# Optimization experiments

Hardware: AMD Instinct MI355X
Metric: run time of the kernel (lower is better)

The kernel has to match this reference:

```python
import jax, jax.numpy as jnp
import numpy as np

B, N, K, D, H, T = 32, 4096, 8, 256, 4, 3
DH = D // H
SCALE = DH ** -0.5
EPS = 1e-8
HID = 256


def layernorm(x, w, b, eps=1e-5):
    m = jnp.mean(x, axis=-1, keepdims=True)
    v = jnp.var(x, axis=-1, keepdims=True)
    return (x - m) * jax.lax.rsqrt(v + eps) * w + b


def setup_inputs() -> dict:
    key = jax.random.key(0)
    ks = jax.random.split(key, 20)
    p = 0.02
    inp = {
        "x": jax.random.normal(ks[0], (B, N, D), jnp.float32),
        "noise": jax.random.normal(ks[1], (B, K, D), jnp.float32),
        "mu": jax.random.normal(ks[2], (1, 1, D), jnp.float32),
        "log_sigma": jax.random.normal(ks[3], (1, 1, D), jnp.float32) * p,
        "norm_in_w": jnp.ones((D,), jnp.float32), "norm_in_b": jnp.zeros((D,), jnp.float32),
        "norm_slot_w": jnp.ones((D,), jnp.float32), "norm_slot_b": jnp.zeros((D,), jnp.float32),
        "norm_mlp_w": jnp.ones((D,), jnp.float32), "norm_mlp_b": jnp.zeros((D,), jnp.float32),
        "Wq": jax.random.normal(ks[4], (D, D), jnp.float32) * p,
        "Wk": jax.random.normal(ks[5], (D, D), jnp.float32) * p,
        "Wv": jax.random.normal(ks[6], (D, D), jnp.float32) * p,
        "Wo": jax.random.normal(ks[7], (D, D), jnp.float32) * p,
        "gru_Wih": jax.random.normal(ks[8], (3 * D, D), jnp.float32) * p,
        "gru_Whh": jax.random.normal(ks[9], (3 * D, D), jnp.float32) * p,
        "gru_bih": jnp.zeros((3 * D,), jnp.float32),
        "gru_bhh": jnp.zeros((3 * D,), jnp.float32),
        "mlp_W1": jax.random.normal(ks[10], (HID, D), jnp.float32) * p,
        "mlp_b1": jnp.zeros((HID,), jnp.float32),
        "mlp_W2": jax.random.normal(ks[11], (D, HID), jnp.float32) * p,
        "mlp_b2": jnp.zeros((D,), jnp.float32),
    }
    return inp


def _split(t):
    # [b, n, D] -> [b, H, n, d_h]
    b, n, _ = t.shape
    return t.reshape(b, n, H, DH).transpose(0, 2, 1, 3)


def _merge(t):
    # [b, H, n, d_h] -> [b, n, D]
    b, h, n, d = t.shape
    return t.transpose(0, 2, 1, 3).reshape(b, n, h * d)


def _step(slots, k_feat, v_feat, p):
    b, k, d = slots.shape
    q = _split(layernorm(slots, p["norm_slot_w"], p["norm_slot_b"]) @ p["Wq"].T)
    dots = jnp.einsum("bhkd,bhnd->bhkn", q, k_feat) * SCALE
    attn = jax.nn.softmax(dots, axis=2)              # softmax over slot (query) axis
    attn = attn / (jnp.sum(attn, axis=-1, keepdims=True) + EPS)  # renorm over keys
    upd = _merge(jnp.einsum("bhkn,bhnd->bhkd", attn, v_feat)) @ p["Wo"].T
    # GRUCell(update, slots)
    gi = upd @ p["gru_Wih"].T + p["gru_bih"]
    gh = slots @ p["gru_Whh"].T + p["gru_bhh"]
    i_r, i_z, i_n = jnp.split(gi, 3, axis=-1)
    h_r, h_z, h_n = jnp.split(gh, 3, axis=-1)
    r = jax.nn.sigmoid(i_r + h_r)
    z = jax.nn.sigmoid(i_z + h_z)
    n = jnp.tanh(i_n + r * h_n)
    slots = (1.0 - z) * n + z * slots
    h1 = jax.nn.relu(layernorm(slots, p["norm_mlp_w"], p["norm_mlp_b"]) @ p["mlp_W1"].T + p["mlp_b1"])
    return slots + h1 @ p["mlp_W2"].T + p["mlp_b2"]


def reference(x, noise, mu, log_sigma, norm_in_w, norm_in_b, norm_slot_w, norm_slot_b,
              norm_mlp_w, norm_mlp_b, Wq, Wk, Wv, Wo, gru_Wih, gru_Whh, gru_bih, gru_bhh,
              mlp_W1, mlp_b1, mlp_W2, mlp_b2):
    p = dict(norm_slot_w=norm_slot_w, norm_slot_b=norm_slot_b, norm_mlp_w=norm_mlp_w,
             norm_mlp_b=norm_mlp_b, Wq=Wq, Wo=Wo, gru_Wih=gru_Wih, gru_Whh=gru_Whh,
             gru_bih=gru_bih, gru_bhh=gru_bhh, mlp_W1=mlp_W1, mlp_b1=mlp_b1,
             mlp_W2=mlp_W2, mlp_b2=mlp_b2)
    slots = mu + jnp.exp(log_sigma) * noise          # [B, K, D]
    xn = layernorm(x, norm_in_w, norm_in_b)
    k_feat = _split(xn @ Wk.T)                       # [B, H, N, d_h]
    v_feat = _split(xn @ Wv.T)
    for _ in range(T):
        slots = _step(slots, k_feat, v_feat, p)
    return slots
```

## Files before the change

kernel.cpp:

```cpp
#include <hip/hip_runtime.h>
#include <stdint.h>

typedef unsigned short ushort_t;
typedef __attribute__((ext_vector_type(8))) short bfrag;
typedef __attribute__((ext_vector_type(4))) float ffrag;

#define B_  32
#define K_  8
#define N_  4096
#define D_  256
#define H_  4
#define DH_ 64

__device__ __forceinline__ ushort_t f2bf(float f) {
  unsigned int u = __builtin_bit_cast(unsigned int, f);
  u += 0x7FFFu + ((u >> 16) & 1u);
  return (ushort_t)(u >> 16);
}

__global__ __launch_bounds__(256) void k_prep_wkv(const float* __restrict__ Wk, const float* __restrict__ Wv,
                                                  const float* __restrict__ lnw, const float* __restrict__ lnb,
                                                  ushort_t* __restrict__ wkv,
                                                  float* __restrict__ c1, float* __restrict__ c2) {
  int n = blockIdx.x;
  int i = threadIdx.x;
  float wv = (n < 256) ? Wk[n*256 + i] : Wv[(n-256)*256 + i];
  float wp = lnw[i] * wv;
  wkv[n*256 + i] = f2bf(wp);
  float p1 = wp, p2 = lnb[i] * wv;
  #pragma unroll
  for (int off = 32; off >= 1; off >>= 1) { p1 += __shfl_xor(p1, off); p2 += __shfl_xor(p2, off); }
  __shared__ float r1[4], r2[4];
  int w = threadIdx.x >> 6;
  if ((threadIdx.x & 63) == 0) { r1[w] = p1; r2[w] = p2; }
  __syncthreads();
  if (threadIdx.x == 0) { c1[n] = r1[0]+r1[1]+r1[2]+r1[3]; c2[n] = r2[0]+r2[1]+r2[2]+r2[3]; }
}

__global__ __launch_bounds__(256) void k_prep_wf(const float* __restrict__ Wih, const float* __restrict__ Wo,
                                                 float* __restrict__ Wf) {
  int j = blockIdx.x;
  int i = threadIdx.x;
  __shared__ float row[256];
  row[i] = Wih[j*256 + i];
  __syncthreads();
  float acc = 0.f;
  #pragma unroll 8
  for (int t = 0; t < 256; ++t) acc += row[t] * Wo[t*256 + i];
  Wf[j*256 + i] = acc;
}

__device__ __forceinline__ void row_ln_256(float (*S)[256], float (*L)[256],
                                           const float* __restrict__ w, const float* __restrict__ b, int t) {
  int k = t >> 5, ln = t & 31;
  float s = 0.f, q = 0.f;
  #pragma unroll
  for (int j = 0; j < 8; ++j) { float v = S[k][ln + j*32]; s += v; q += v*v; }
  #pragma unroll
  for (int off = 16; off >= 1; off >>= 1) { s += __shfl_xor(s, off); q += __shfl_xor(q, off); }
  float m = s * (1.f/256.f);
  float rstd = rsqrtf(q * (1.f/256.f) - m*m + 1e-5f);
  #pragma unroll
  for (int j = 0; j < 8; ++j) {
    int c = ln + j*32;
    L[k][c] = (S[k][c] - m) * rstd * w[c] + b[c];
  }
}

__device__ __forceinline__ void qproj(float (*L)[256], const float* __restrict__ Wq,
                                      ushort_t* __restrict__ qbuf, int b, int t) {
  int c = t;
  const float4* Wrow = (const float4*)(Wq + (size_t)c * 256);
  float acc[8];
  #pragma unroll
  for (int k = 0; k < 8; ++k) acc[k] = 0.f;
  for (int i = 0; i < 64; ++i) {
    float4 wv = Wrow[i];
    #pragma unroll
    for (int k = 0; k < 8; ++k) {
      float4 xv = *((const float4*)&L[k][0] + i);
      acc[k] = fmaf(xv.x, wv.x, fmaf(xv.y, wv.y, fmaf(xv.z, wv.z, fmaf(xv.w, wv.w, acc[k]))));
    }
  }
  int h = c >> 6, dh = c & 63;
  ushort_t* dst = qbuf + ((size_t)(b*4 + h) * 16) * 64 + dh;
  #pragma unroll
  for (int k = 0; k < 8; ++k) dst[k*64] = f2bf(acc[k] * 0.125f);
  #pragma unroll
  for (int k = 8; k < 16; ++k) dst[k*64] = 0;
}

__device__ __forceinline__ void row_ln_4x(float (*S)[256], float (*L)[256],
                                          const float* __restrict__ w, const float* __restrict__ b, int t) {
  int k = t >> 6, ln = t & 63;
  float s = 0.f, q = 0.f;
  #pragma unroll
  for (int j = 0; j < 4; ++j) { float v = S[k][ln + j*64]; s += v; q += v*v; }
  #pragma unroll
  for (int off = 32; off >= 1; off >>= 1) { s += __shfl_xor(s, off); q += __shfl_xor(q, off); }
  float m = s * (1.f/256.f);
  float rstd = rsqrtf(q * (1.f/256.f) - m*m + 1e-5f);
  #pragma unroll
  for (int j = 0; j < 4; ++j) {
    int c = ln + j*64;
    L[k][c] = (S[k][c] - m) * rstd * w[c] + b[c];
  }
}

__device__ __forceinline__ void qproj4(float (*L)[256], const float* __restrict__ Wq,
                                       ushort_t* __restrict__ qbuf, int b, int ks0, int t) {
  int c = t;
  const float4* Wrow = (const float4*)(Wq + (size_t)c * 256);
  float acc[4];
  #pragma unroll
  for (int k = 0; k < 4; ++k) acc[k] = 0.f;
  for (int i = 0; i < 64; ++i) {
    float4 wv = Wrow[i];
    #pragma unroll
    for (int k = 0; k < 4; ++k) {
      float4 xv = *((const float4*)&L[k][0] + i);
      acc[k] = fmaf(xv.x, wv.x, fmaf(xv.y, wv.y, fmaf(xv.z, wv.z, fmaf(xv.w, wv.w, acc[k]))));
    }
  }
  int h = c >> 6, dh = c & 63;
  ushort_t* dst = qbuf + ((size_t)(b*4 + h) * 16) * 64 + dh;
  #pragma unroll
  for (int k = 0; k < 4; ++k) dst[(ks0 + k)*64] = f2bf(acc[k] * 0.125f);
  #pragma unroll
  for (int k = 0; k < 4; ++k) dst[(8 + ks0 + k)*64] = 0;
}

__global__ __launch_bounds__(256) void k_init(const float* __restrict__ noise, const float* __restrict__ mu,
                                              const float* __restrict__ lsig, float* __restrict__ slots,
                                              const float* __restrict__ nsw, const float* __restrict__ nsb,
                                              const float* __restrict__ Wq, ushort_t* __restrict__ qbuf) {
  int b = blockIdx.x, t = threadIdx.x;
  __shared__ float S[8][256];
  __shared__ float L[8][256];
  float e = __expf(lsig[t]);
  float m = mu[t];
  #pragma unroll
  for (int k = 0; k < 8; ++k) {
    float v = m + e * noise[((size_t)(b*8+k))*256 + t];
    S[k][t] = v;
    slots[((size_t)(b*8+k))*256 + t] = v;
  }
  __syncthreads();
  row_ln_256(S, L, nsw, nsb, t);
  __syncthreads();
  qproj(L, Wq, qbuf, b, t);
}

__global__ __launch_bounds__(256, 3) void k_gemm(const float* __restrict__ x,
                                                 const ushort_t* __restrict__ wkv,
                                                 const float* __restrict__ c1, const float* __restrict__ c2,
                                                 ushort_t* __restrict__ kf, ushort_t* __restrict__ vfT) {
  int mb = blockIdx.x, cb = blockIdx.y;
  int t = threadIdx.x, w = t >> 6, l = t & 63;
  __shared__ uint4 ldsv[2048];
  char* lds = (char*)ldsv;
  const int m0 = mb * 128, col0 = cb * 128;
  int r0 = t >> 1, half = t & 1;

  float4 xa[4];
  uint4 wb[2];
  float ssum = 0.f, sqsum = 0.f;
  int swzW = ((r0 >> 1) & 3) << 4;

  auto loadA = [&](int s) {
    const float4* src = (const float4*)(x + (size_t)(m0 + r0) * 256 + s*32 + half*16);
    #pragma unroll
    for (int i = 0; i < 4; ++i) xa[i] = src[i];
  };
  auto loadB = [&](int s) {
    const uint4* src = (const uint4*)(wkv + (size_t)(col0 + r0) * 256 + s*32 + half*16);
    wb[0] = src[0]; wb[1] = src[1];
  };
  auto writeA = [&](char* Ab) {
    #pragma unroll
    for (int i = 0; i < 2; ++i) {
      float4 a = xa[2*i], b2 = xa[2*i+1];
      ssum  += a.x + a.y + a.z + a.w + b2.x + b2.y + b2.z + b2.w;
      sqsum += a.x*a.x + a.y*a.y + a.z*a.z + a.w*a.w
             + b2.x*b2.x + b2.y*b2.y + b2.z*b2.z + b2.w*b2.w;
      union { ushort_t us[8]; uint4 v; } u;
      u.us[0]=f2bf(a.x);  u.us[1]=f2bf(a.y);  u.us[2]=f2bf(a.z);  u.us[3]=f2bf(a.w);
      u.us[4]=f2bf(b2.x); u.us[5]=f2bf(b2.y); u.us[6]=f2bf(b2.z); u.us[7]=f2bf(b2.w);
      *(uint4*)(Ab + r0*64 + ((half*32 + i*16) ^ swzW)) = u.v;
    }
  };
  auto writeB = [&](char* Bb) {
    #pragma unroll
    for (int i = 0; i < 2; ++i)
      *(uint4*)(Bb + r0*64 + ((half*32 + i*16) ^ swzW)) = wb[i];
  };

  ffrag acc[4][4];
  #pragma unroll
  for (int i = 0; i < 4; ++i)
    #pragma unroll
    for (int j = 0; j < 4; ++j) acc[i][j] = (ffrag){0.f,0.f,0.f,0.f};

  int wm = w & 1, wn = w >> 1;
  int lrow = l & 15, lkb = ((l >> 4) * 8) * 2;

  loadA(0); loadB(0);
  writeA(lds); writeB(lds + 16384);
  __syncthreads();

  for (int s = 0; s < 8; ++s) {
    char* Ac = lds + ((s & 1) << 13);
    char* Bc = lds + 16384 + ((s & 1) << 13);
    if (s < 7) { loadA(s+1); loadB(s+1); }
    bfrag bfr[4];
    #pragma unroll
    for (int j = 0; j < 4; ++j) {
      int row = wn*64 + j*16 + lrow;
      bfr[j] = *(const bfrag*)(Bc + row*64 + (lkb ^ (((row >> 1) & 3) << 4)));
    }
    #pragma unroll
    for (int i = 0; i < 4; ++i) {
      int row = wm*64 + i*16 + lrow;
      bfrag afr = *(const bfrag*)(Ac + row*64 + (lkb ^ (((row >> 1) & 3) << 4)));
      #pragma unroll
      for (int j = 0; j < 4; ++j)
        acc[i][j] = __builtin_amdgcn_mfma_f32_16x16x32_bf16(afr, bfr[j], acc[i][j], 0, 0, 0);
    }
    if (s < 7) {
      char* An = lds + (((s+1) & 1) << 13);
      char* Bn = lds + 16384 + (((s+1) & 1) << 13);
      writeA(An); writeB(Bn);
    }
    __syncthreads();
  }

  float s2 = ssum  + __shfl_xor(ssum, 1);
  float q2 = sqsum + __shfl_xor(sqsum, 1);
  float* statm = (float*)(lds + 28672);
  float* statr = (float*)(lds + 29184);
  if (half == 0) {
    float mm = s2 * (1.f/256.f);
    statm[r0] = mm;
    statr[r0] = rsqrtf(q2 * (1.f/256.f) - mm*mm + 1e-5f);
  }
  __syncthreads();

  int g = l >> 4, nl = l & 15;
  int b = m0 >> 12, nx0 = m0 & 4095;
  if (cb < 2) {
    for (int p = 0; p < 2; ++p) {
      if (wm == p) {
        #pragma unroll
        for (int i = 0; i < 4; ++i) {
          #pragma unroll
          for (int j = 0; j < 4; ++j) {
            int coll = wn*64 + j*16 + nl;
            float cc1 = c1[col0 + coll], cc2 = c2[col0 + coll];
            #pragma unroll
            for (int r = 0; r < 4; ++r) {
              int ml = i*16 + g*4 + r;
              int mlg = p*64 + ml;
              float val = statr[mlg] * (acc[i][j][r] - statm[mlg] * cc1) + cc2;
              *(ushort_t*)(lds + (ml*136 + coll)*2) = f2bf(val);
            }
          }
        }
      }
      __syncthreads();
      {
        int mloc = t >> 2, hh = (t >> 1) & 1, qq = t & 1;
        int h = cb*2 + hh;
        ushort_t* dst = kf + ((size_t)((b*4 + h)*4096 + nx0 + p*64 + mloc)) * 64 + qq*32;
        const char* srcr = lds + mloc*272 + hh*128 + qq*64;
        #pragma unroll
        for (int jj = 0; jj < 4; ++jj)
          ((uint4*)dst)[jj] = *(const uint4*)(srcr + jj*16);
      }
      __syncthreads();
    }
  } else {
    for (int p = 0; p < 2; ++p) {
      if (wn == p) {
        #pragma unroll
        for (int i = 0; i < 4; ++i) {
          int mlb = wm*64 + i*16 + g*4;
          #pragma unroll
          for (int j = 0; j < 4; ++j) {
            int coll = j*16 + nl;
            int collg = p*64 + coll;
            float cc1 = c1[col0 + collg], cc2 = c2[col0 + collg];
            ushort_t us[4];
            #pragma unroll
            for (int r = 0; r < 4; ++r)
              us[r] = f2bf(statr[mlb+r] * (acc[i][j][r] - statm[mlb+r] * cc1) + cc2);
            *(uint2*)(lds + coll*272 + mlb*2) =
              make_uint2((unsigned)us[0] | ((unsigned)us[1] << 16),
                         (unsigned)us[2] | ((unsigned)us[3] << 16));
          }
        }
      }
      __syncthreads();
      {
        int cl = t >> 2, seg = t & 3;
        int collg = p*64 + cl;
        int h = (cb - 2)*2 + (collg >> 6);
        int dh = collg & 63;
        ushort_t* dst = vfT + ((size_t)((b*4 + h)*64 + dh)) * 4096 + nx0 + seg*32;
        const char* srcr = lds + cl*272 + seg*64;
        #pragma unroll
        for (int jj = 0; jj < 4; ++jj)
          ((uint4*)dst)[jj] = *(const uint4*)(srcr + jj*16);
      }
      __syncthreads();
    }
  }
}

__global__ __launch_bounds__(256, 4) void k_attn(const ushort_t* __restrict__ q, const ushort_t* __restrict__ kf,
                                                 const ushort_t* __restrict__ vfT,
                                                 float* __restrict__ updp, float* __restrict__ asump) {
  int split = blockIdx.x;
  int bh = blockIdx.y;
  int n0 = split * 256;
  int t = threadIdx.x, w = t >> 6, l = t & 63;
  __shared__ uint4 ldsv[640];
  char* lds = (char*)ldsv;
  char* Pl = lds;
  char* Ql = lds + 8192;

  if (t < 128) {
    int k = t >> 3, seg = t & 7;
    uint4 v = *(const uint4*)(q + ((size_t)bh*16 + k) * 64 + seg*8);
    *(uint4*)(Ql + k*128 + ((seg*16) ^ ((k & 7) << 4))) = v;
  }
  *(uint4*)(Pl + 4096 + t*16) = make_uint4(0,0,0,0);
  __syncthreads();

  int g = l >> 4, nl = l & 15, lk = g * 8;
  const ushort_t* kbase = kf + ((size_t)bh*4096 + n0) * 64;

  ffrag dacc[4];
  #pragma unroll
  for (int nt = 0; nt < 4; ++nt) {
    dacc[nt] = (ffrag){0.f,0.f,0.f,0.f};
    int row = w*64 + nt*16 + nl;
    #pragma unroll
    for (int kk = 0; kk < 2; ++kk) {
      bfrag af = *(const bfrag*)(Ql + nl*128 + (((kk*32 + lk)*2) ^ ((nl & 7) << 4)));
      bfrag bf = *(const bfrag*)(kbase + (size_t)row*64 + kk*32 + lk);
      dacc[nt] = __builtin_amdgcn_mfma_f32_16x16x32_bf16(af, bf, dacc[nt], 0, 0, 0);
    }
  }

  float asr0 = 0.f, asr1 = 0.f, asr2 = 0.f, asr3 = 0.f;
  #pragma unroll
  for (int nt = 0; nt < 4; ++nt) {
    float d0 = dacc[nt][0], d1 = dacc[nt][1], d2 = dacc[nt][2], d3 = dacc[nt][3];
    float mx = fmaxf(fmaxf(d0, d1), fmaxf(d2, d3));
    mx = fmaxf(mx, __shfl_xor(mx, 16));
    float p0 = __expf(d0 - mx), p1 = __expf(d1 - mx), p2 = __expf(d2 - mx), p3 = __expf(d3 - mx);
    float sden = p0 + p1 + p2 + p3;
    sden += __shfl_xor(sden, 16);
    float inv = 1.f / sden;
    p0 *= inv; p1 *= inv; p2 *= inv; p3 *= inv;
    if (g < 2) {
      asr0 += p0; asr1 += p1; asr2 += p2; asr3 += p3;
      int n = w*64 + nt*16 + nl;
      int k0 = g*4;
      *(ushort_t*)(Pl + (((k0+0)*512 + n*2) ^ (((k0+0)&7) << 4))) = f2bf(p0);
      *(ushort_t*)(Pl + (((k0+1)*512 + n*2) ^ (((k0+1)&7) << 4))) = f2bf(p1);
      *(ushort_t*)(Pl + (((k0+2)*512 + n*2) ^ (((k0+2)&7) << 4))) = f2bf(p2);
      *(ushort_t*)(Pl + (((k0+3)*512 + n*2) ^ (((k0+3)&7) << 4))) = f2bf(p3);
    }
  }
  #pragma unroll
  for (int off = 8; off >= 1; off >>= 1) {
    asr0 += __shfl_xor(asr0, off); asr1 += __shfl_xor(asr1, off);
    asr2 += __shfl_xor(asr2, off); asr3 += __shfl_xor(asr3, off);
  }
  if (g < 2 && nl == 0) {
    float* dst = asump + (((size_t)bh*16 + split)*4 + w)*8 + g*4;
    dst[0] = asr0; dst[1] = asr1; dst[2] = asr2; dst[3] = asr3;
  }
  __syncthreads();

  const ushort_t* vbase = vfT + ((size_t)bh*64) * 4096 + n0;
  ffrag pacc = (ffrag){0.f,0.f,0.f,0.f};
  int d = w*16 + nl;
  #pragma unroll
  for (int ni = 0; ni < 8; ++ni) {
    int nn = ni * 32;
    bfrag af = *(const bfrag*)(Pl + nl*512 + (((nn + lk)*2) ^ ((nl & 7) << 4)));
    bfrag bf = *(const bfrag*)(vbase + (size_t)d*4096 + nn + lk);
    pacc = __builtin_amdgcn_mfma_f32_16x16x32_bf16(af, bf, pacc, 0, 0, 0);
  }
  if (g < 2) {
    float* dst = updp + (((size_t)bh*16 + split)*8 + g*4)*64 + w*16 + nl;
    #pragma unroll
    for (int r = 0; r < 4; ++r) dst[r*64] = pacc[r];
  }
}

__global__ __launch_bounds__(256) void k_u1(const float* __restrict__ updp, const float* __restrict__ asump,
                                            const float* __restrict__ slots,
                                            const float* __restrict__ Wf, const float* __restrict__ Whh,
                                            const float* __restrict__ bih, const float* __restrict__ bhh,
                                            float* __restrict__ gi, float* __restrict__ gh) {
  int cb = blockIdx.x, b = blockIdx.y, t = threadIdx.x;
  int c = cb * 256 + t;
  bool isGi = (c < 768);
  __shared__ float X[8][256];
  __shared__ float asumS[4][8];
  if (isGi) {
    if (t < 32) {
      int h = t >> 3, kk = t & 7;
      const float* ap = asump + (size_t)(b*4 + h) * 512;
      float a = 0.f;
      #pragma unroll
      for (int s = 0; s < 64; ++s) a += ap[s*8 + kk];
      asumS[h][kk] = a + 1e-8f;
    }
    __syncthreads();
    int h = t >> 6, d = t & 63;
    const float* up = updp + (size_t)(b*4 + h) * 8192 + d;
    #pragma unroll
    for (int k = 0; k < 8; ++k) {
      float u = 0.f;
      #pragma unroll
      for (int s = 0; s < 16; ++s) u += up[s*512 + k*64];
      X[k][t] = u / asumS[h][k];
    }
  } else {
    #pragma unroll
    for (int k = 0; k < 8; ++k) X[k][t] = slots[((size_t)(b*8+k))*256 + t];
  }
  __syncthreads();
  int cc = isGi ? c : (c - 768);
  const float* Wrow = (isGi ? Wf : Whh) + (size_t)cc * 256;
  float bias = isGi ? bih[cc] : bhh[cc];
  float acc[8];
  #pragma unroll
  for (int k = 0; k < 8; ++k) acc[k] = bias;
  for (int i = 0; i < 64; ++i) {
    float4 wv = ((const float4*)Wrow)[i];
    #pragma unroll
    for (int k = 0; k < 8; ++k) {
      float4 xv = *((const float4*)&X[k][0] + i);
      acc[k] = fmaf(xv.x, wv.x, fmaf(xv.y, wv.y, fmaf(xv.z, wv.z, fmaf(xv.w, wv.w, acc[k]))));
    }
  }
  float* dst = isGi ? gi : gh;
  #pragma unroll
  for (int k = 0; k < 8; ++k) dst[((size_t)(b*8+k))*768 + cc] = acc[k];
}

__global__ __launch_bounds__(256) void k_u2(const float* __restrict__ gi, const float* __restrict__ gh,
                                            const float* __restrict__ slots_in, float* __restrict__ slots_out,
                                            const float* __restrict__ nmw, const float* __restrict__ nmb,
                                            const float* __restrict__ W1, const float* __restrict__ b1,
                                            const float* __restrict__ W2, const float* __restrict__ b2,
                                            const float* __restrict__ nsw, const float* __restrict__ nsb,
                                            const float* __restrict__ Wq, ushort_t* __restrict__ qbuf, int do_q) {
  int bid = blockIdx.x;
  int b = bid >> 1, ks0 = (bid & 1) * 4;
  int t = threadIdx.x;
  __shared__ float S[4][256];
  __shared__ float L[4][256];
  __shared__ float H1[4][256];
  #pragma unroll
  for (int k = 0; k < 4; ++k) {
    int slot = b*8 + ks0 + k;
    size_t gb = (size_t)slot * 768;
    float ir = gi[gb + t],        hr = gh[gb + t];
    float iz = gi[gb + 256 + t],  hz = gh[gb + 256 + t];
    float in_ = gi[gb + 512 + t], hn = gh[gb + 512 + t];
    float r = 1.f / (1.f + __expf(-(ir + hr)));
    float z = 1.f / (1.f + __expf(-(iz + hz)));
    float a = in_ + r * hn;
    float e2 = __expf(-2.f * fabsf(a));
    float nn = (1.f - e2) / (1.f + e2);
    nn = copysignf(nn, a);
    S[k][t] = (1.f - z) * nn + z * slots_in[(size_t)slot * 256 + t];
  }
  __syncthreads();
  row_ln_4x(S, L, nmw, nmb, t);
  __syncthreads();
  {
    const float4* Wrow = (const float4*)(W1 + (size_t)t * 256);
    float bb = b1[t];
    float acc[4];
    #pragma unroll
    for (int k = 0; k < 4; ++k) acc[k] = bb;
    for (int i = 0; i < 64; ++i) {
      float4 wv = Wrow[i];
      #pragma unroll
      for (int k = 0; k < 4; ++k) {
        float4 xv = *((const float4*)&L[k][0] + i);
        acc[k] = fmaf(xv.x, wv.x, fmaf(xv.y, wv.y, fmaf(xv.z, wv.z, fmaf(xv.w, wv.w, acc[k]))));
      }
    }
    #pragma unroll
    for (int k = 0; k < 4; ++k) H1[k][t] = fmaxf(acc[k], 0.f);
  }
  __syncthreads();
  {
    const float4* Wrow = (const float4*)(W2 + (size_t)t * 256);
    float bb = b2[t];
    float acc[4];
    #pragma unroll
    for (int k = 0; k < 4; ++k) acc[k] = bb;
    for (int i = 0; i < 64; ++i) {
      float4 wv = Wrow[i];
      #pragma unroll
      for (int k = 0; k < 4; ++k) {
        float4 xv = *((const float4*)&H1[k][0] + i);
        acc[k] = fmaf(xv.x, wv.x, fmaf(xv.y, wv.y, fmaf(xv.z, wv.z, fmaf(xv.w, wv.w, acc[k]))));
      }
    }
    #pragma unroll
    for (int k = 0; k < 4; ++k) {
      int slot = b*8 + ks0 + k;
      float o = S[k][t] + acc[k];
      slots_out[(size_t)slot * 256 + t] = o;
      S[k][t] = o;
    }
  }
  __syncthreads();
  if (do_q) {
    row_ln_4x(S, L, nsw, nsb, t);
    __syncthreads();
    qproj4(L, Wq, qbuf, b, ks0, t);
  }
}

extern "C" void kernel_launch(void* const* d_in, const int* in_sizes, int n_in,
                              void* d_out, int out_size, void* d_ws, size_t ws_size,
                              hipStream_t stream) {
  (void)in_sizes; (void)n_in; (void)out_size; (void)ws_size;
  const float* x     = (const float*)d_in[0];
  const float* noise = (const float*)d_in[1];
  const float* mu    = (const float*)d_in[2];
  const float* lsig  = (const float*)d_in[3];
  const float* ninw  = (const float*)d_in[4];
  const float* ninb  = (const float*)d_in[5];
  const float* nsw   = (const float*)d_in[6];
  const float* nsb   = (const float*)d_in[7];
  const float* nmw   = (const float*)d_in[8];
  const float* nmb   = (const float*)d_in[9];
  const float* Wq    = (const float*)d_in[10];
  const float* Wk    = (const float*)d_in[11];
  const float* Wv    = (const float*)d_in[12];
  const float* Wo    = (const float*)d_in[13];
  const float* Wih   = (const float*)d_in[14];
  const float* Whh   = (const float*)d_in[15];
  const float* bih   = (const float*)d_in[16];
  const float* bhh   = (const float*)d_in[17];
  const float* W1    = (const float*)d_in[18];
  const float* b1    = (const float*)d_in[19];
  const float* W2    = (const float*)d_in[20];
  const float* b2    = (const float*)d_in[21];

  char* ws = (char*)d_ws;
  ushort_t* wkv   = (ushort_t*)(ws + 0);
  float*    c1    = (float*)   (ws + 262144);
  float*    c2    = (float*)   (ws + 264192);
  float*    Wf    = (float*)   (ws + 266240);
  float*    slots = (float*)   (ws + 1052672);
  ushort_t* qbuf  = (ushort_t*)(ws + 1314816);
  float*    gi    = (float*)   (ws + 1839104);
  float*    gh    = (float*)   (ws + 2625536);
  float*    asump = (float*)   (ws + 3411968);
  float*    updp  = (float*)   (ws + 3674112);
  ushort_t* kf    = (ushort_t*)(ws + 7868416);
  ushort_t* vfT   = (ushort_t*)(ws + 74977280);

  k_prep_wkv<<<512,          256, 0, stream>>>(Wk, Wv, ninw, ninb, wkv, c1, c2);
  k_gemm    <<<dim3(1024,4), 256, 0, stream>>>(x, wkv, c1, c2, kf, vfT);
  k_prep_wf <<<768,          256, 0, stream>>>(Wih, Wo, Wf);
  k_init    <<<32,           256, 0, stream>>>(noise, mu, lsig, slots, nsw, nsb, Wq, qbuf);

  float* outp = (float*)d_out;
  for (int it = 0; it < 3; ++it) {
    k_attn<<<dim3(16, 128), 256, 0, stream>>>(qbuf, kf, vfT, updp, asump);
    k_u1  <<<dim3(6, 32),   256, 0, stream>>>(updp, asump, slots, Wf, Whh, bih, bhh, gi, gh);
    k_u2  <<<64,            256, 0, stream>>>(gi, gh, slots, (it == 2) ? outp : slots,
                                              nmw, nmb, W1, b1, W2, b2, nsw, nsb, Wq, qbuf, (it < 2) ? 1 : 0);
  }
}
```

Before: 591.5 us.

## Stage GEMM weight tiles via direct global-to-LDS loads and regroup block order

The B (bf16 weight) operand of the K/V projection GEMM is now copied straight from global memory into LDS with the global_load_lds builtin, replacing the register round-trip, and a permuted source column order preserves the XOR swizzle. The 2D grid is flattened to 1D and remapped so the four column blocks of each 64-row-block chunk are scheduled together, aiming for better L2 reuse of the x rows. This frees registers and VALU work, but it relies on the direct-to-LDS write layout matching the swizzled reads, and synchronisation of the async loads depends on the existing barrier.

```diff
diff --git a/kernel.cpp b/kernel.cpp
--- a/kernel.cpp
+++ b/kernel.cpp
@@ -16,6 +16,12 @@
   unsigned int u = __builtin_bit_cast(unsigned int, f);
   u += 0x7FFFu + ((u >> 16) & 1u);
   return (ushort_t)(u >> 16);
+}
+
+__device__ __forceinline__ void gload_lds16(const void* g, void* l) {
+  __builtin_amdgcn_global_load_lds((const __attribute__((address_space(1))) unsigned int*)g,
+                                   (__attribute__((address_space(3))) unsigned int*)l,
+                                   16, 0, 0);
 }
 
 __global__ __launch_bounds__(256) void k_prep_wkv(const float* __restrict__ Wk, const float* __restrict__ Wv,
@@ -155,7 +161,11 @@
                                                  const ushort_t* __restrict__ wkv,
                                                  const float* __restrict__ c1, const float* __restrict__ c2,
                                                  ushort_t* __restrict__ kf, ushort_t* __restrict__ vfT) {
-  int mb = blockIdx.x, cb = blockIdx.y;
+  int wg = blockIdx.x;
+  int chunk = wg >> 8;
+  int within = wg & 255;
+  int cb = within >> 6;
+  int mb = (chunk << 6) | (within & 63);
   int t = threadIdx.x, w = t >> 6, l = t & 63;
   __shared__ uint4 ldsv[2048];
   char* lds = (char*)ldsv;
@@ -163,7 +173,6 @@
   int r0 = t >> 1, half = t & 1;
 
   float4 xa[4];
-  uint4 wb[2];
   float ssum = 0.f, sqsum = 0.f;
   int swzW = ((r0 >> 1) & 3) << 4;
 
@@ -171,10 +180,6 @@
     const float4* src = (const float4*)(x + (size_t)(m0 + r0) * 256 + s*32 + half*16);
     #pragma unroll
     for (int i = 0; i < 4; ++i) xa[i] = src[i];
-  };
-  auto loadB = [&](int s) {
-    const uint4* src = (const uint4*)(wkv + (size_t)(col0 + r0) * 256 + s*32 + half*16);
-    wb[0] = src[0]; wb[1] = src[1];
   };
   auto writeA = [&](char* Ab) {
     #pragma unroll
@@ -189,10 +194,16 @@
       *(uint4*)(Ab + r0*64 + ((half*32 + i*16) ^ swzW)) = u.v;
     }
   };
-  auto writeB = [&](char* Bb) {
-    #pragma unroll
-    for (int i = 0; i < 2; ++i)
-      *(uint4*)(Bb + r0*64 + ((half*32 + i*16) ^ swzW)) = wb[i];
+  int rB0 = (l >> 2);
+  int permB = ((l & 3) ^ ((rB0 >> 1) & 3)) * 8;
+  auto stageB = [&](int buf, int s) {
+    char* Bb = lds + 16384 + (buf << 13);
+    #pragma unroll
+    for (int j = 0; j < 2; ++j) {
+      int row = (w*2 + j)*16 + rB0;
+      const ushort_t* src = wkv + (size_t)(col0 + row)*256 + s*32 + permB;
+      gload_lds16(src, Bb + (w*2 + j)*1024);
+    }
   };
 
   ffrag acc[4][4];
@@ -204,14 +215,14 @@
   int wm = w & 1, wn = w >> 1;
   int lrow = l & 15, lkb = ((l >> 4) * 8) * 2;
 
-  loadA(0); loadB(0);
-  writeA(lds); writeB(lds + 16384);
+  loadA(0); writeA(lds);
+  stageB(0, 0);
   __syncthreads();
 
   for (int s = 0; s < 8; ++s) {
     char* Ac = lds + ((s & 1) << 13);
     char* Bc = lds + 16384 + ((s & 1) << 13);
-    if (s < 7) { loadA(s+1); loadB(s+1); }
+    if (s < 7) { loadA(s+1); stageB((s+1) & 1, s+1); }
     bfrag bfr[4];
     #pragma unroll
     for (int j = 0; j < 4; ++j) {
@@ -228,8 +239,7 @@
     }
     if (s < 7) {
       char* An = lds + (((s+1) & 1) << 13);
-      char* Bn = lds + 16384 + (((s+1) & 1) << 13);
-      writeA(An); writeB(Bn);
+      writeA(An);
     }
     __syncthreads();
   }
@@ -574,10 +584,10 @@
   ushort_t* kf    = (ushort_t*)(ws + 7868416);
   ushort_t* vfT   = (ushort_t*)(ws + 74977280);
 
-  k_prep_wkv<<<512,          256, 0, stream>>>(Wk, Wv, ninw, ninb, wkv, c1, c2);
-  k_gemm    <<<dim3(1024,4), 256, 0, stream>>>(x, wkv, c1, c2, kf, vfT);
-  k_prep_wf <<<768,          256, 0, stream>>>(Wih, Wo, Wf);
-  k_init    <<<32,           256, 0, stream>>>(noise, mu, lsig, slots, nsw, nsb, Wq, qbuf);
+  k_prep_wkv<<<512,  256, 0, stream>>>(Wk, Wv, ninw, ninb, wkv, c1, c2);
+  k_gemm    <<<4096, 256, 0, stream>>>(x, wkv, c1, c2, kf, vfT);
+  k_prep_wf <<<768,  256, 0, stream>>>(Wih, Wo, Wf);
+  k_init    <<<32,   256, 0, stream>>>(noise, mu, lsig, slots, nsw, nsb, Wq, qbuf);
 
   float* outp = (float*)d_out;
   for (int it = 0; it < 3; ++it) {
```

New measurement: 609.3 us. 3.0% more time.
